# Kernel optimization log

Measured on AMD Instinct MI355X. Metric: run time of the kernel, lower is better.

Reference implementation:

```python
import jax, jax.numpy as jnp
import numpy as np

N_NODES = 100000
N_EDGES = 1250000
D_IN, D_HID, D_OUT = 64, 32, 41


def setup_inputs() -> dict:
    key = jax.random.key(0)
    ks = jax.random.split(key, 7)
    x = jax.random.normal(ks[0], (N_NODES, D_IN), dtype=jnp.float32)
    edge_index = jax.random.randint(ks[1], (2, N_EDGES), 0, N_NODES, dtype=jnp.int64)
    # PyG SAGEConv params: lin_l (applied to aggregated neighbors, has bias),
    # lin_r (applied to root, no bias). Stored here as [in, out] matrices.
    W1l = jax.random.normal(ks[2], (D_IN, D_HID), dtype=jnp.float32) / np.sqrt(D_IN)
    b1 = jnp.zeros((D_HID,), dtype=jnp.float32)
    W1r = jax.random.normal(ks[3], (D_IN, D_HID), dtype=jnp.float32) / np.sqrt(D_IN)
    W2l = jax.random.normal(ks[4], (D_HID, D_OUT), dtype=jnp.float32) / np.sqrt(D_HID)
    b2 = jnp.zeros((D_OUT,), dtype=jnp.float32)
    W2r = jax.random.normal(ks[5], (D_HID, D_OUT), dtype=jnp.float32) / np.sqrt(D_HID)
    return {"x": x, "edge_index": edge_index, "W1l": W1l, "b1": b1, "W1r": W1r,
            "W2l": W2l, "b2": b2, "W2r": W2r}


def _sage_conv(h, src, dst, n_nodes, Wl, b, Wr):
    # mean-aggregate source features at destination nodes (PyG default aggr='mean')
    msg = h[src]  # [E, d] irregular gather
    agg = jax.ops.segment_sum(msg, dst, num_segments=n_nodes)
    cnt = jax.ops.segment_sum(jnp.ones((src.shape[0],), dtype=h.dtype), dst,
                              num_segments=n_nodes)
    agg = agg / jnp.maximum(cnt, 1.0)[:, None]
    return agg @ Wl + b + h @ Wr


def reference(x, edge_index, W1l, b1, W1r, W2l, b2, W2r):
    src, dst = edge_index[0], edge_index[1]
    n = x.shape[0]
    h = _sage_conv(x, src, dst, n, W1l, b1, W1r)
    h = jax.nn.relu(h)
    # F.dropout(training=self.training) -> identity in eval/inference mode
    out = _sage_conv(h, src, dst, n, W2l, b2, W2r)
    return out
```

## Files before the change

kernel.cpp:

```cpp
#include <hip/hip_runtime.h>

#define N_NODES 100000
#define N_EDGES 1250000
#define D_IN 64
#define D_HID 32
#define D_OUT 41
#define NBUK 196
#define BSH 9
#define BCAP 6912
#define BBLK 512
#define BCHUNK 2442
#define PBLK 1563
#define ROWCAP 48
#define LSTR 88
#define ZERO_OFF 6400000

typedef short bf16x8 __attribute__((ext_vector_type(8)));
typedef float f32x4 __attribute__((ext_vector_type(4)));

__device__ __forceinline__ float bflo(unsigned int u) {
    union { unsigned int i; float f; } v; v.i = u << 16; return v.f;
}
__device__ __forceinline__ float bfhi(unsigned int u) {
    union { unsigned int i; float f; } v; v.i = u & 0xffff0000u; return v.f;
}
__device__ __forceinline__ unsigned short f2bf(float f) {
    union { float f; unsigned int i; } v; v.f = f;
    unsigned int x = v.i;
    return (unsigned short)((x + 0x7fffu + ((x >> 16) & 1u)) >> 16);
}
__device__ __forceinline__ void acc8(float* a, uint4 u) {
    a[0] += bflo(u.x); a[1] += bfhi(u.x);
    a[2] += bflo(u.y); a[3] += bfhi(u.y);
    a[4] += bflo(u.z); a[5] += bfhi(u.z);
    a[6] += bflo(u.w); a[7] += bfhi(u.w);
}

__global__ __launch_bounds__(256) void k_front(const int* __restrict__ src,
                                               const int* __restrict__ dst,
                                               unsigned int* __restrict__ bucket_cnt,
                                               unsigned int* __restrict__ buckets,
                                               const float* __restrict__ x,
                                               const float* __restrict__ W1l,
                                               const float* __restrict__ W1r,
                                               const float* __restrict__ b1,
                                               unsigned short* __restrict__ xl,
                                               unsigned short* __restrict__ xr) {
    __shared__ short smem[2 * 64 * LSTR];
    int tid = threadIdx.x;
    if (blockIdx.x < BBLK) {
        int* hist = (int*)smem;
        int* cur  = hist + NBUK;
        for (int i = tid; i < NBUK; i += 256)
            atomicCAS(&bucket_cnt[i], 0xAAAAAAAAu, 0u);
        for (int i = tid; i < NBUK; i += 256) hist[i] = 0;
        __syncthreads();
        int e0 = blockIdx.x * BCHUNK;
        int e1 = e0 + BCHUNK; if (e1 > N_EDGES) e1 = N_EDGES;
        int e = e0 + tid;
        for (; e + 768 < e1; e += 1024) {
            int t0 = dst[e];
            int t1 = dst[e + 256];
            int t2 = dst[e + 512];
            int t3 = dst[e + 768];
            atomicAdd(&hist[t0 >> BSH], 1);
            atomicAdd(&hist[t1 >> BSH], 1);
            atomicAdd(&hist[t2 >> BSH], 1);
            atomicAdd(&hist[t3 >> BSH], 1);
        }
        for (; e < e1; e += 256)
            atomicAdd(&hist[dst[e] >> BSH], 1);
        __syncthreads();
        for (int i = tid; i < NBUK; i += 256)
            cur[i] = (int)atomicAdd(&bucket_cnt[i], (unsigned int)hist[i]);
        __syncthreads();
        e = e0 + tid;
        for (; e + 768 < e1; e += 1024) {
            int t0 = dst[e],       s0 = src[e];
            int t1 = dst[e + 256], s1 = src[e + 256];
            int t2 = dst[e + 512], s2 = src[e + 512];
            int t3 = dst[e + 768], s3 = src[e + 768];
            int b0 = t0 >> BSH, p0 = atomicAdd(&cur[b0], 1);
            if (p0 < BCAP) buckets[(size_t)b0 * BCAP + p0] =
                (unsigned int)s0 | ((unsigned int)(t0 & 511) << 17);
            int b1i = t1 >> BSH, p1 = atomicAdd(&cur[b1i], 1);
            if (p1 < BCAP) buckets[(size_t)b1i * BCAP + p1] =
                (unsigned int)s1 | ((unsigned int)(t1 & 511) << 17);
            int b2 = t2 >> BSH, p2 = atomicAdd(&cur[b2], 1);
            if (p2 < BCAP) buckets[(size_t)b2 * BCAP + p2] =
                (unsigned int)s2 | ((unsigned int)(t2 & 511) << 17);
            int b3 = t3 >> BSH, p3 = atomicAdd(&cur[b3], 1);
            if (p3 < BCAP) buckets[(size_t)b3 * BCAP + p3] =
                (unsigned int)s3 | ((unsigned int)(t3 & 511) << 17);
        }
        for (; e < e1; e += 256) {
            int t = dst[e];
            int b = t >> BSH;
            int pos = atomicAdd(&cur[b], 1);
            if (pos < BCAP)
                buckets[(size_t)b * BCAP + pos] =
                    (unsigned int)src[e] | ((unsigned int)(t & 511) << 17);
        }
        return;
    }
    short* sX  = smem;
    short* sWT = smem + 64 * LSTR;
    int n0 = (blockIdx.x - BBLK) * 64;
    for (int i = tid; i < 64 * 64; i += 256) {
        int col = i >> 6, kk = i & 63;
        float v = (col < 32) ? W1l[kk * 32 + col] : W1r[kk * 32 + (col - 32)];
        sWT[col * LSTR + kk] = (short)f2bf(v);
    }
    {
        int g = tid >> 2, q = tid & 3;
        int n = n0 + g;
        short pk[16];
        if (n < N_NODES) {
            const float4* xr4 = (const float4*)(x + (size_t)n * D_IN + q * 16);
            float4 f0 = xr4[0], f1 = xr4[1], f2 = xr4[2], f3 = xr4[3];
            pk[0] = f2bf(f0.x); pk[1] = f2bf(f0.y); pk[2] = f2bf(f0.z); pk[3] = f2bf(f0.w);
            pk[4] = f2bf(f1.x); pk[5] = f2bf(f1.y); pk[6] = f2bf(f1.z); pk[7] = f2bf(f1.w);
            pk[8] = f2bf(f2.x); pk[9] = f2bf(f2.y); pk[10] = f2bf(f2.z); pk[11] = f2bf(f2.w);
            pk[12] = f2bf(f3.x); pk[13] = f2bf(f3.y); pk[14] = f2bf(f3.z); pk[15] = f2bf(f3.w);
        } else {
            for (int t = 0; t < 16; ++t) pk[t] = 0;
        }
        *(bf16x8*)(sX + g * LSTR + q * 16)     = *(bf16x8*)pk;
        *(bf16x8*)(sX + g * LSTR + q * 16 + 8) = *(bf16x8*)(pk + 8);
    }
    __syncthreads();
    int wid = tid >> 6, lane = tid & 63;
    int quad = lane >> 4, lc = lane & 15;
    int m0 = wid << 4;
    const short* sa = sX + (m0 + lc) * LSTR + quad * 8;
    bf16x8 af0 = *(const bf16x8*)(sa);
    bf16x8 af1 = *(const bf16x8*)(sa + 32);
#pragma unroll
    for (int t = 0; t < 4; ++t) {
        const short* sbp = sWT + (t * 16 + lc) * LSTR + quad * 8;
        bf16x8 bf0 = *(const bf16x8*)(sbp);
        bf16x8 bf1 = *(const bf16x8*)(sbp + 32);
        f32x4 acc = {0.f, 0.f, 0.f, 0.f};
        acc = __builtin_amdgcn_mfma_f32_16x16x32_bf16(af0, bf0, acc, 0, 0, 0);
        acc = __builtin_amdgcn_mfma_f32_16x16x32_bf16(af1, bf1, acc, 0, 0, 0);
        int col = t * 16 + lc;
        float bias = (col >= 32) ? b1[col - 32] : 0.f;
#pragma unroll
        for (int r = 0; r < 4; ++r) {
            int n = n0 + m0 + (quad << 2) + r;
            if (n < N_NODES) {
                if (col < 32) xl[(size_t)n * D_HID + col] = f2bf(acc[r]);
                else          xr[(size_t)n * D_HID + (col - 32)] = f2bf(acc[r] + bias);
            } else if (col < 32) {
                xl[(size_t)n * D_HID + col] = 0;
            }
        }
    }
}

__global__ __launch_bounds__(256) void k_fill2(const unsigned int* __restrict__ buckets,
                                               const unsigned int* __restrict__ bucket_cnt,
                                               int* __restrict__ cnt,
                                               int* __restrict__ padcsr) {
    __shared__ int lcnt[512];
    int b = blockIdx.x, tid = threadIdx.x;
    lcnt[tid] = 0; lcnt[tid + 256] = 0;
    __syncthreads();
    int total = (int)bucket_cnt[b]; if (total > BCAP) total = BCAP;
    const unsigned int* bk = buckets + (size_t)b * BCAP;
    int nbase = b << BSH;
    int i = tid;
    for (; i + 768 < total; i += 1024) {
        unsigned int w0 = bk[i];
        unsigned int w1 = bk[i + 256];
        unsigned int w2 = bk[i + 512];
        unsigned int w3 = bk[i + 768];
        int d0 = (int)(w0 >> 17), s0 = atomicAdd(&lcnt[d0], 1);
        if (s0 < ROWCAP) padcsr[(size_t)(nbase + d0) * ROWCAP + s0] = (int)((w0 & 0x1FFFFu) << 6);
        int d1 = (int)(w1 >> 17), s1 = atomicAdd(&lcnt[d1], 1);
        if (s1 < ROWCAP) padcsr[(size_t)(nbase + d1) * ROWCAP + s1] = (int)((w1 & 0x1FFFFu) << 6);
        int d2 = (int)(w2 >> 17), s2 = atomicAdd(&lcnt[d2], 1);
        if (s2 < ROWCAP) padcsr[(size_t)(nbase + d2) * ROWCAP + s2] = (int)((w2 & 0x1FFFFu) << 6);
        int d3 = (int)(w3 >> 17), s3 = atomicAdd(&lcnt[d3], 1);
        if (s3 < ROWCAP) padcsr[(size_t)(nbase + d3) * ROWCAP + s3] = (int)((w3 & 0x1FFFFu) << 6);
    }
    for (; i < total; i += 256) {
        unsigned int w = bk[i];
        int dl = (int)(w >> 17);
        int slot = atomicAdd(&lcnt[dl], 1);
        if (slot < ROWCAP)
            padcsr[(size_t)(nbase + dl) * ROWCAP + slot] = (int)((w & 0x1FFFFu) << 6);
    }
    __syncthreads();
#pragma unroll
    for (int half = 0; half < 2; ++half) {
        int li = tid + half * 256;
        int n = nbase + li;
        int c = lcnt[li];
        cnt[n] = c;
        int cc = c < ROWCAP ? c : ROWCAP;
        int ce = (cc + 15) & ~15; if (ce > ROWCAP) ce = ROWCAP;
        for (int s = cc; s < ce; ++s)
            padcsr[(size_t)n * ROWCAP + s] = ZERO_OFF;
    }
}

__global__ __launch_bounds__(256) void k_agg1(const int* __restrict__ padcsr,
                                              const int* __restrict__ cnt,
                                              const unsigned short* __restrict__ xl,
                                              const unsigned short* __restrict__ xr,
                                              unsigned short* __restrict__ h) {
    int tid = threadIdx.x;
    int g = tid >> 2, q = tid & 3;
    int n = blockIdx.x * 64 + g;
    int qb = q << 4;
    if (n >= N_NODES) {
        *(uint4*)((char*)h + ((size_t)n << 6) + qb) = make_uint4(0, 0, 0, 0);
        return;
    }
    int d = cnt[n];
    int dd = d < ROWCAP ? d : ROWCAP;
    int ddp = (dd + 15) & ~15; if (ddp > ROWCAP) ddp = ROWCAP;
    const int* row = padcsr + (size_t)n * ROWCAP;
    const char* xlb = (const char*)xl;
    float a[8] = {0.f, 0.f, 0.f, 0.f, 0.f, 0.f, 0.f, 0.f};
    for (int i = 0; i < ddp; i += 16) {
        int4 o0 = *(const int4*)(row + i);
        int4 o1 = *(const int4*)(row + i + 4);
        int4 o2 = *(const int4*)(row + i + 8);
        int4 o3 = *(const int4*)(row + i + 12);
        uint4 u0 = *(const uint4*)(xlb + o0.x + qb);
        uint4 u1 = *(const uint4*)(xlb + o0.y + qb);
        uint4 u2 = *(const uint4*)(xlb + o0.z + qb);
        uint4 u3 = *(const uint4*)(xlb + o0.w + qb);
        uint4 u4 = *(const uint4*)(xlb + o1.x + qb);
        uint4 u5 = *(const uint4*)(xlb + o1.y + qb);
        uint4 u6 = *(const uint4*)(xlb + o1.z + qb);
        uint4 u7 = *(const uint4*)(xlb + o1.w + qb);
        uint4 u8 = *(const uint4*)(xlb + o2.x + qb);
        uint4 u9 = *(const uint4*)(xlb + o2.y + qb);
        uint4 ua = *(const uint4*)(xlb + o2.z + qb);
        uint4 ub = *(const uint4*)(xlb + o2.w + qb);
        uint4 uc = *(const uint4*)(xlb + o3.x + qb);
        uint4 ud = *(const uint4*)(xlb + o3.y + qb);
        uint4 ue = *(const uint4*)(xlb + o3.z + qb);
        uint4 uf = *(const uint4*)(xlb + o3.w + qb);
        acc8(a, u0); acc8(a, u1); acc8(a, u2); acc8(a, u3);
        acc8(a, u4); acc8(a, u5); acc8(a, u6); acc8(a, u7);
        acc8(a, u8); acc8(a, u9); acc8(a, ua); acc8(a, ub);
        acc8(a, uc); acc8(a, ud); acc8(a, ue); acc8(a, uf);
    }
    float inv = 1.0f / fmaxf((float)d, 1.0f);
    uint4 r = *(const uint4*)((const char*)xr + ((size_t)n << 6) + qb);
    float o0 = fmaxf(a[0] * inv + bflo(r.x), 0.f);
    float o1 = fmaxf(a[1] * inv + bfhi(r.x), 0.f);
    float o2 = fmaxf(a[2] * inv + bflo(r.y), 0.f);
    float o3 = fmaxf(a[3] * inv + bfhi(r.y), 0.f);
    float o4 = fmaxf(a[4] * inv + bflo(r.z), 0.f);
    float o5 = fmaxf(a[5] * inv + bfhi(r.z), 0.f);
    float o6 = fmaxf(a[6] * inv + bflo(r.w), 0.f);
    float o7 = fmaxf(a[7] * inv + bfhi(r.w), 0.f);
    uint4 o;
    o.x = ((unsigned int)f2bf(o1) << 16) | f2bf(o0);
    o.y = ((unsigned int)f2bf(o3) << 16) | f2bf(o2);
    o.z = ((unsigned int)f2bf(o5) << 16) | f2bf(o4);
    o.w = ((unsigned int)f2bf(o7) << 16) | f2bf(o6);
    *(uint4*)((char*)h + ((size_t)n << 6) + qb) = o;
}

__global__ __launch_bounds__(256) void k_agg2out(const int* __restrict__ padcsr,
                                                 const int* __restrict__ cnt,
                                                 const unsigned short* __restrict__ h,
                                                 const float* __restrict__ W2l,
                                                 const float* __restrict__ b2,
                                                 const float* __restrict__ W2r,
                                                 float* __restrict__ out) {
    __shared__ short sA[64 * LSTR];
    __shared__ short sBT[48 * LSTR];
    int tid = threadIdx.x;
    int n0 = blockIdx.x * 64;
    for (int i = tid; i < 48 * 64; i += 256) {
        int col = i >> 6, kk = i & 63;
        float v = 0.f;
        if (col < D_OUT) v = (kk < 32) ? W2l[kk * D_OUT + col] : W2r[(kk - 32) * D_OUT + col];
        sBT[col * LSTR + kk] = (short)f2bf(v);
    }
    {
        int g = tid >> 2, q = tid & 3;
        int n = n0 + g;
        bool ok = (n < N_NODES);
        int qb = q << 4;
        int d = ok ? cnt[n] : 0;
        int dd = d < ROWCAP ? d : ROWCAP;
        int ddp = (dd + 15) & ~15; if (ddp > ROWCAP) ddp = ROWCAP;
        const int* row = padcsr + (size_t)n * ROWCAP;
        const char* hb = (const char*)h;
        float a[8] = {0.f, 0.f, 0.f, 0.f, 0.f, 0.f, 0.f, 0.f};
        for (int i = 0; i < ddp; i += 16) {
            int4 o0 = *(const int4*)(row + i);
            int4 o1 = *(const int4*)(row + i + 4);
            int4 o2 = *(const int4*)(row + i + 8);
            int4 o3 = *(const int4*)(row + i + 12);
            uint4 u0 = *(const uint4*)(hb + o0.x + qb);
            uint4 u1 = *(const uint4*)(hb + o0.y + qb);
            uint4 u2 = *(const uint4*)(hb + o0.z + qb);
            uint4 u3 = *(const uint4*)(hb + o0.w + qb);
            uint4 u4 = *(const uint4*)(hb + o1.x + qb);
            uint4 u5 = *(const uint4*)(hb + o1.y + qb);
            uint4 u6 = *(const uint4*)(hb + o1.z + qb);
            uint4 u7 = *(const uint4*)(hb + o1.w + qb);
            uint4 u8 = *(const uint4*)(hb + o2.x + qb);
            uint4 u9 = *(const uint4*)(hb + o2.y + qb);
            uint4 ua = *(const uint4*)(hb + o2.z + qb);
            uint4 ub = *(const uint4*)(hb + o2.w + qb);
            uint4 uc = *(const uint4*)(hb + o3.x + qb);
            uint4 ud = *(const uint4*)(hb + o3.y + qb);
            uint4 ue = *(const uint4*)(hb + o3.z + qb);
            uint4 uf = *(const uint4*)(hb + o3.w + qb);
            acc8(a, u0); acc8(a, u1); acc8(a, u2); acc8(a, u3);
            acc8(a, u4); acc8(a, u5); acc8(a, u6); acc8(a, u7);
            acc8(a, u8); acc8(a, u9); acc8(a, ua); acc8(a, ub);
            acc8(a, uc); acc8(a, ud); acc8(a, ue); acc8(a, uf);
        }
        float inv = 1.0f / fmaxf((float)d, 1.0f);
        short pk[8];
#pragma unroll
        for (int t = 0; t < 8; ++t) pk[t] = (short)f2bf(a[t] * inv);
        *(bf16x8*)(sA + g * LSTR + q * 8) = *(bf16x8*)pk;
        uint4 hr = ok ? *(const uint4*)(hb + ((size_t)n << 6) + qb)
                      : make_uint4(0, 0, 0, 0);
        *(uint4*)(sA + g * LSTR + 32 + q * 8) = hr;
    }
    __syncthreads();
    int wid = tid >> 6, lane = tid & 63;
    int quad = lane >> 4, lc = lane & 15;
    int m0 = wid << 4;
    const short* sa = sA + (m0 + lc) * LSTR + quad * 8;
    bf16x8 af0 = *(const bf16x8*)(sa);
    bf16x8 af1 = *(const bf16x8*)(sa + 32);
#pragma unroll
    for (int t = 0; t < 3; ++t) {
        const short* sbp = sBT + (t * 16 + lc) * LSTR + quad * 8;
        bf16x8 bf0 = *(const bf16x8*)(sbp);
        bf16x8 bf1 = *(const bf16x8*)(sbp + 32);
        f32x4 acc = {0.f, 0.f, 0.f, 0.f};
        acc = __builtin_amdgcn_mfma_f32_16x16x32_bf16(af0, bf0, acc, 0, 0, 0);
        acc = __builtin_amdgcn_mfma_f32_16x16x32_bf16(af1, bf1, acc, 0, 0, 0);
        int j = t * 16 + lc;
        if (j < D_OUT) {
            float bias = b2[j];
#pragma unroll
            for (int r = 0; r < 4; ++r) {
                int n = n0 + m0 + (quad << 2) + r;
                if (n < N_NODES) out[(size_t)n * D_OUT + j] = acc[r] + bias;
            }
        }
    }
}

extern "C" void kernel_launch(void* const* d_in, const int* in_sizes, int n_in,
                              void* d_out, int out_size, void* d_ws, size_t ws_size,
                              hipStream_t stream) {
    const float* x   = (const float*)d_in[0];
    const int*   ei  = (const int*)d_in[1];
    const int*   src = ei;
    const int*   dst = ei + N_EDGES;
    const float* W1l = (const float*)d_in[2];
    const float* b1  = (const float*)d_in[3];
    const float* W1r = (const float*)d_in[4];
    const float* W2l = (const float*)d_in[5];
    const float* b2  = (const float*)d_in[6];
    const float* W2r = (const float*)d_in[7];
    float* out = (float*)d_out;

    int* iws = (int*)d_ws;
    int* cnt        = iws;
    unsigned int* bucket_cnt = (unsigned int*)(iws + 100352);
    int* padcsr     = iws + 100608;
    unsigned int* buckets = (unsigned int*)(iws + 4917504);
    unsigned short* xl = (unsigned short*)(iws + 6272256);
    unsigned short* xr = (unsigned short*)(iws + 7872768);
    unsigned short* h  = (unsigned short*)(iws + 9473280);

    k_front<<<BBLK + PBLK, 256, 0, stream>>>(src, dst, bucket_cnt, buckets,
                                             x, W1l, W1r, b1, xl, xr);
    k_fill2<<<NBUK, 256, 0, stream>>>(buckets, bucket_cnt, cnt, padcsr);
    k_agg1<<<1563, 256, 0, stream>>>(padcsr, cnt, xl, xr, h);
    k_agg2out<<<1563, 256, 0, stream>>>(padcsr, cnt, h, W2l, b2, W2r, out);
}
```

Baseline: 189.5 us.

## Aggregate directly from dst buckets with LDS atomics, dropping padded CSR build

```diff
diff --git a/kernel.cpp b/kernel.cpp
--- a/kernel.cpp
+++ b/kernel.cpp
@@ -5,15 +5,14 @@
 #define D_IN 64
 #define D_HID 32
 #define D_OUT 41
-#define NBUK 196
-#define BSH 9
-#define BCAP 6912
-#define BBLK 512
-#define BCHUNK 2442
-#define PBLK 1563
-#define ROWCAP 48
+#define NBUK 784
+#define BSH 7
+#define BCAP 1920
+#define BBLK 192
+#define BCHUNK 6511
+#define PBLK 782
 #define LSTR 88
-#define ZERO_OFF 6400000
+#define ASTR 33
 
 typedef short bf16x8 __attribute__((ext_vector_type(8)));
 typedef float f32x4 __attribute__((ext_vector_type(4)));
@@ -29,11 +28,39 @@
     unsigned int x = v.i;
     return (unsigned short)((x + 0x7fffu + ((x >> 16) & 1u)) >> 16);
 }
-__device__ __forceinline__ void acc8(float* a, uint4 u) {
-    a[0] += bflo(u.x); a[1] += bfhi(u.x);
-    a[2] += bflo(u.y); a[3] += bfhi(u.y);
-    a[4] += bflo(u.z); a[5] += bfhi(u.z);
-    a[6] += bflo(u.w); a[7] += bfhi(u.w);
+
+__device__ __forceinline__ void ds_add8(float* accL, int* degL, unsigned int w,
+                                        uint4 u, int q) {
+    int dl = (int)(w >> 17);
+    float* p = accL + dl * ASTR + q * 8;
+    atomicAdd(p + 0, bflo(u.x)); atomicAdd(p + 1, bfhi(u.x));
+    atomicAdd(p + 2, bflo(u.y)); atomicAdd(p + 3, bfhi(u.y));
+    atomicAdd(p + 4, bflo(u.z)); atomicAdd(p + 5, bfhi(u.z));
+    atomicAdd(p + 6, bflo(u.w)); atomicAdd(p + 7, bfhi(u.w));
+    if (q == 0) atomicAdd(degL + dl, 1);
+}
+
+__device__ __forceinline__ void scan_accumulate(const unsigned int* bk, int total,
+                                                const char* tab, float* accL,
+                                                int* degL, int tid) {
+    int g = tid >> 2, q = tid & 3, qb = q << 4;
+    int t = g;
+    for (; t + 192 < total; t += 256) {
+        unsigned int w0 = bk[t], w1 = bk[t + 64], w2 = bk[t + 128], w3 = bk[t + 192];
+        uint4 u0 = *(const uint4*)(tab + ((w0 & 0x1FFFFu) << 6) + qb);
+        uint4 u1 = *(const uint4*)(tab + ((w1 & 0x1FFFFu) << 6) + qb);
+        uint4 u2 = *(const uint4*)(tab + ((w2 & 0x1FFFFu) << 6) + qb);
+        uint4 u3 = *(const uint4*)(tab + ((w3 & 0x1FFFFu) << 6) + qb);
+        ds_add8(accL, degL, w0, u0, q);
+        ds_add8(accL, degL, w1, u1, q);
+        ds_add8(accL, degL, w2, u2, q);
+        ds_add8(accL, degL, w3, u3, q);
+    }
+    for (; t < total; t += 64) {
+        unsigned int w = bk[t];
+        uint4 u = *(const uint4*)(tab + ((w & 0x1FFFFu) << 6) + qb);
+        ds_add8(accL, degL, w, u, q);
+    }
 }
 
 __global__ __launch_bounds__(256) void k_front(const int* __restrict__ src,
@@ -46,13 +73,11 @@
                                                const float* __restrict__ b1,
                                                unsigned short* __restrict__ xl,
                                                unsigned short* __restrict__ xr) {
-    __shared__ short smem[2 * 64 * LSTR];
+    __shared__ short smem[128 * LSTR + 64 * LSTR];
     int tid = threadIdx.x;
     if (blockIdx.x < BBLK) {
         int* hist = (int*)smem;
         int* cur  = hist + NBUK;
-        for (int i = tid; i < NBUK; i += 256)
-            atomicCAS(&bucket_cnt[i], 0xAAAAAAAAu, 0u);
         for (int i = tid; i < NBUK; i += 256) hist[i] = 0;
         __syncthreads();
         int e0 = blockIdx.x * BCHUNK;
@@ -72,7 +97,7 @@
             atomicAdd(&hist[dst[e] >> BSH], 1);
         __syncthreads();
         for (int i = tid; i < NBUK; i += 256)
-            cur[i] = (int)atomicAdd(&bucket_cnt[i], (unsigned int)hist[i]);
+            cur[i] = (int)atomicAdd(&bucket_cnt[i << 4], (unsigned int)hist[i]);
         __syncthreads();
         e = e0 + tid;
         for (; e + 768 < e1; e += 1024) {
@@ -82,16 +107,16 @@
             int t3 = dst[e + 768], s3 = src[e + 768];
             int b0 = t0 >> BSH, p0 = atomicAdd(&cur[b0], 1);
             if (p0 < BCAP) buckets[(size_t)b0 * BCAP + p0] =
-                (unsigned int)s0 | ((unsigned int)(t0 & 511) << 17);
+                (unsigned int)s0 | ((unsigned int)(t0 & 127) << 17);
             int b1i = t1 >> BSH, p1 = atomicAdd(&cur[b1i], 1);
             if (p1 < BCAP) buckets[(size_t)b1i * BCAP + p1] =
-                (unsigned int)s1 | ((unsigned int)(t1 & 511) << 17);
+                (unsigned int)s1 | ((unsigned int)(t1 & 127) << 17);
             int b2 = t2 >> BSH, p2 = atomicAdd(&cur[b2], 1);
             if (p2 < BCAP) buckets[(size_t)b2 * BCAP + p2] =
-                (unsigned int)s2 | ((unsigned int)(t2 & 511) << 17);
+                (unsigned int)s2 | ((unsigned int)(t2 & 127) << 17);
             int b3 = t3 >> BSH, p3 = atomicAdd(&cur[b3], 1);
             if (p3 < BCAP) buckets[(size_t)b3 * BCAP + p3] =
-                (unsigned int)s3 | ((unsigned int)(t3 & 511) << 17);
+                (unsigned int)s3 | ((unsigned int)(t3 & 127) << 17);
         }
         for (; e < e1; e += 256) {
             int t = dst[e];
@@ -99,262 +124,189 @@
             int pos = atomicAdd(&cur[b], 1);
             if (pos < BCAP)
                 buckets[(size_t)b * BCAP + pos] =
-                    (unsigned int)src[e] | ((unsigned int)(t & 511) << 17);
+                    (unsigned int)src[e] | ((unsigned int)(t & 127) << 17);
         }
         return;
     }
     short* sX  = smem;
-    short* sWT = smem + 64 * LSTR;
-    int n0 = (blockIdx.x - BBLK) * 64;
-    for (int i = tid; i < 64 * 64; i += 256) {
-        int col = i >> 6, kk = i & 63;
-        float v = (col < 32) ? W1l[kk * 32 + col] : W1r[kk * 32 + (col - 32)];
-        sWT[col * LSTR + kk] = (short)f2bf(v);
+    short* sWT = smem + 128 * LSTR;
+    int n0 = (blockIdx.x - BBLK) * 128;
+    for (int i = tid; i < 1024; i += 256) {
+        int k = i >> 4, c4 = i & 15;
+        float4 v = (c4 < 8) ? ((const float4*)W1l)[k * 8 + c4]
+                            : ((const float4*)W1r)[k * 8 + (c4 - 8)];
+        int col = c4 * 4;
+        sWT[(col + 0) * LSTR + k] = (short)f2bf(v.x);
+        sWT[(col + 1) * LSTR + k] = (short)f2bf(v.y);
+        sWT[(col + 2) * LSTR + k] = (short)f2bf(v.z);
+        sWT[(col + 3) * LSTR + k] = (short)f2bf(v.w);
     }
     {
-        int g = tid >> 2, q = tid & 3;
+        int g = tid >> 1, q2 = tid & 1;
         int n = n0 + g;
-        short pk[16];
+        short pk[32];
         if (n < N_NODES) {
-            const float4* xr4 = (const float4*)(x + (size_t)n * D_IN + q * 16);
-            float4 f0 = xr4[0], f1 = xr4[1], f2 = xr4[2], f3 = xr4[3];
-            pk[0] = f2bf(f0.x); pk[1] = f2bf(f0.y); pk[2] = f2bf(f0.z); pk[3] = f2bf(f0.w);
-            pk[4] = f2bf(f1.x); pk[5] = f2bf(f1.y); pk[6] = f2bf(f1.z); pk[7] = f2bf(f1.w);
-            pk[8] = f2bf(f2.x); pk[9] = f2bf(f2.y); pk[10] = f2bf(f2.z); pk[11] = f2bf(f2.w);
-            pk[12] = f2bf(f3.x); pk[13] = f2bf(f3.y); pk[14] = f2bf(f3.z); pk[15] = f2bf(f3.w);
+            const float4* xp = (const float4*)(x + (size_t)n * D_IN + q2 * 32);
+#pragma unroll
+            for (int i = 0; i < 8; ++i) {
+                float4 f = xp[i];
+                pk[i * 4 + 0] = (short)f2bf(f.x);
+                pk[i * 4 + 1] = (short)f2bf(f.y);
+                pk[i * 4 + 2] = (short)f2bf(f.z);
+                pk[i * 4 + 3] = (short)f2bf(f.w);
+            }
         } else {
-            for (int t = 0; t < 16; ++t) pk[t] = 0;
-        }
-        *(bf16x8*)(sX + g * LSTR + q * 16)     = *(bf16x8*)pk;
-        *(bf16x8*)(sX + g * LSTR + q * 16 + 8) = *(bf16x8*)(pk + 8);
+#pragma unroll
+            for (int i = 0; i < 32; ++i) pk[i] = 0;
+        }
+        short* sp = sX + g * LSTR + q2 * 32;
+        *(bf16x8*)(sp)      = *(bf16x8*)(pk);
+        *(bf16x8*)(sp + 8)  = *(bf16x8*)(pk + 8);
+        *(bf16x8*)(sp + 16) = *(bf16x8*)(pk + 16);
+        *(bf16x8*)(sp + 24) = *(bf16x8*)(pk + 24);
     }
     __syncthreads();
     int wid = tid >> 6, lane = tid & 63;
     int quad = lane >> 4, lc = lane & 15;
-    int m0 = wid << 4;
-    const short* sa = sX + (m0 + lc) * LSTR + quad * 8;
-    bf16x8 af0 = *(const bf16x8*)(sa);
-    bf16x8 af1 = *(const bf16x8*)(sa + 32);
-#pragma unroll
-    for (int t = 0; t < 4; ++t) {
-        const short* sbp = sWT + (t * 16 + lc) * LSTR + quad * 8;
-        bf16x8 bf0 = *(const bf16x8*)(sbp);
-        bf16x8 bf1 = *(const bf16x8*)(sbp + 32);
-        f32x4 acc = {0.f, 0.f, 0.f, 0.f};
-        acc = __builtin_amdgcn_mfma_f32_16x16x32_bf16(af0, bf0, acc, 0, 0, 0);
-        acc = __builtin_amdgcn_mfma_f32_16x16x32_bf16(af1, bf1, acc, 0, 0, 0);
-        int col = t * 16 + lc;
-        float bias = (col >= 32) ? b1[col - 32] : 0.f;
-#pragma unroll
-        for (int r = 0; r < 4; ++r) {
-            int n = n0 + m0 + (quad << 2) + r;
-            if (n < N_NODES) {
-                if (col < 32) xl[(size_t)n * D_HID + col] = f2bf(acc[r]);
-                else          xr[(size_t)n * D_HID + (col - 32)] = f2bf(acc[r] + bias);
-            } else if (col < 32) {
-                xl[(size_t)n * D_HID + col] = 0;
+#pragma unroll
+    for (int mm = 0; mm < 2; ++mm) {
+        int m0 = (wid + mm * 4) * 16;
+        const short* sa = sX + (m0 + lc) * LSTR + quad * 8;
+        bf16x8 af0 = *(const bf16x8*)(sa);
+        bf16x8 af1 = *(const bf16x8*)(sa + 32);
+#pragma unroll
+        for (int t = 0; t < 4; ++t) {
+            const short* sbp = sWT + (t * 16 + lc) * LSTR + quad * 8;
+            bf16x8 bf0 = *(const bf16x8*)(sbp);
+            bf16x8 bf1 = *(const bf16x8*)(sbp + 32);
+            f32x4 acc = {0.f, 0.f, 0.f, 0.f};
+            acc = __builtin_amdgcn_mfma_f32_16x16x32_bf16(af0, bf0, acc, 0, 0, 0);
+            acc = __builtin_amdgcn_mfma_f32_16x16x32_bf16(af1, bf1, acc, 0, 0, 0);
+            int col = t * 16 + lc;
+            float bias = (col >= 32) ? b1[col - 32] : 0.f;
+#pragma unroll
+            for (int r = 0; r < 4; ++r) {
+                int n = n0 + m0 + (quad << 2) + r;
+                if (n < N_NODES) {
+                    if (col < 32) xl[(size_t)n * D_HID + col] = f2bf(acc[r]);
+                    else          xr[(size_t)n * D_HID + (col - 32)] = f2bf(acc[r] + bias);
+                }
             }
         }
     }
 }
 
-__global__ __launch_bounds__(256) void k_fill2(const unsigned int* __restrict__ buckets,
+__global__ __launch_bounds__(256) void k_bagg1(const unsigned int* __restrict__ buckets,
                                                const unsigned int* __restrict__ bucket_cnt,
-                                               int* __restrict__ cnt,
-                                               int* __restrict__ padcsr) {
-    __shared__ int lcnt[512];
-    int b = blockIdx.x, tid = threadIdx.x;
-    lcnt[tid] = 0; lcnt[tid + 256] = 0;
-    __syncthreads();
-    int total = (int)bucket_cnt[b]; if (total > BCAP) total = BCAP;
-    const unsigned int* bk = buckets + (size_t)b * BCAP;
+                                               const unsigned short* __restrict__ xl,
+                                               const unsigned short* __restrict__ xr,
+                                               unsigned short* __restrict__ h) {
+    __shared__ float accL[128 * ASTR];
+    __shared__ int degL[128];
+    int tid = threadIdx.x, b = blockIdx.x;
+    for (int i = tid; i < 128 * ASTR; i += 256) accL[i] = 0.f;
+    if (tid < 128) degL[tid] = 0;
+    __syncthreads();
+    int total = (int)bucket_cnt[b << 4]; if (total > BCAP) total = BCAP;
+    scan_accumulate(buckets + (size_t)b * BCAP, total, (const char*)xl,
+                    accL, degL, tid);
+    __syncthreads();
     int nbase = b << BSH;
-    int i = tid;
-    for (; i + 768 < total; i += 1024) {
-        unsigned int w0 = bk[i];
-        unsigned int w1 = bk[i + 256];
-        unsigned int w2 = bk[i + 512];
-        unsigned int w3 = bk[i + 768];
-        int d0 = (int)(w0 >> 17), s0 = atomicAdd(&lcnt[d0], 1);
-        if (s0 < ROWCAP) padcsr[(size_t)(nbase + d0) * ROWCAP + s0] = (int)((w0 & 0x1FFFFu) << 6);
-        int d1 = (int)(w1 >> 17), s1 = atomicAdd(&lcnt[d1], 1);
-        if (s1 < ROWCAP) padcsr[(size_t)(nbase + d1) * ROWCAP + s1] = (int)((w1 & 0x1FFFFu) << 6);
-        int d2 = (int)(w2 >> 17), s2 = atomicAdd(&lcnt[d2], 1);
-        if (s2 < ROWCAP) padcsr[(size_t)(nbase + d2) * ROWCAP + s2] = (int)((w2 & 0x1FFFFu) << 6);
-        int d3 = (int)(w3 >> 17), s3 = atomicAdd(&lcnt[d3], 1);
-        if (s3 < ROWCAP) padcsr[(size_t)(nbase + d3) * ROWCAP + s3] = (int)((w3 & 0x1FFFFu) << 6);
-    }
-    for (; i < total; i += 256) {
-        unsigned int w = bk[i];
-        int dl = (int)(w >> 17);
-        int slot = atomicAdd(&lcnt[dl], 1);
-        if (slot < ROWCAP)
-            padcsr[(size_t)(nbase + dl) * ROWCAP + slot] = (int)((w & 0x1FFFFu) << 6);
-    }
-    __syncthreads();
-#pragma unroll
-    for (int half = 0; half < 2; ++half) {
-        int li = tid + half * 256;
+    int q = tid & 3, qb = q << 4;
+#pragma unroll
+    for (int r0 = 0; r0 < 2; ++r0) {
+        int li = (tid >> 2) + r0 * 64;
         int n = nbase + li;
-        int c = lcnt[li];
-        cnt[n] = c;
-        int cc = c < ROWCAP ? c : ROWCAP;
-        int ce = (cc + 15) & ~15; if (ce > ROWCAP) ce = ROWCAP;
-        for (int s = cc; s < ce; ++s)
-            padcsr[(size_t)n * ROWCAP + s] = ZERO_OFF;
-    }
-}
-
-__global__ __launch_bounds__(256) void k_agg1(const int* __restrict__ padcsr,
-                                              const int* __restrict__ cnt,
-                                              const unsigned short* __restrict__ xl,
-                                              const unsigned short* __restrict__ xr,
-                                              unsigned short* __restrict__ h) {
-    int tid = threadIdx.x;
-    int g = tid >> 2, q = tid & 3;
-    int n = blockIdx.x * 64 + g;
-    int qb = q << 4;
-    if (n >= N_NODES) {
-        *(uint4*)((char*)h + ((size_t)n << 6) + qb) = make_uint4(0, 0, 0, 0);
-        return;
-    }
-    int d = cnt[n];
-    int dd = d < ROWCAP ? d : ROWCAP;
-    int ddp = (dd + 15) & ~15; if (ddp > ROWCAP) ddp = ROWCAP;
-    const int* row = padcsr + (size_t)n * ROWCAP;
-    const char* xlb = (const char*)xl;
-    float a[8] = {0.f, 0.f, 0.f, 0.f, 0.f, 0.f, 0.f, 0.f};
-    for (int i = 0; i < ddp; i += 16) {
-        int4 o0 = *(const int4*)(row + i);
-        int4 o1 = *(const int4*)(row + i + 4);
-        int4 o2 = *(const int4*)(row + i + 8);
-        int4 o3 = *(const int4*)(row + i + 12);
-        uint4 u0 = *(const uint4*)(xlb + o0.x + qb);
-        uint4 u1 = *(const uint4*)(xlb + o0.y + qb);
-        uint4 u2 = *(const uint4*)(xlb + o0.z + qb);
-        uint4 u3 = *(const uint4*)(xlb + o0.w + qb);
-        uint4 u4 = *(const uint4*)(xlb + o1.x + qb);
-        uint4 u5 = *(const uint4*)(xlb + o1.y + qb);
-        uint4 u6 = *(const uint4*)(xlb + o1.z + qb);
-        uint4 u7 = *(const uint4*)(xlb + o1.w + qb);
-        uint4 u8 = *(const uint4*)(xlb + o2.x + qb);
-        uint4 u9 = *(const uint4*)(xlb + o2.y + qb);
-        uint4 ua = *(const uint4*)(xlb + o2.z + qb);
-        uint4 ub = *(const uint4*)(xlb + o2.w + qb);
-        uint4 uc = *(const uint4*)(xlb + o3.x + qb);
-        uint4 ud = *(const uint4*)(xlb + o3.y + qb);
-        uint4 ue = *(const uint4*)(xlb + o3.z + qb);
-        uint4 uf = *(const uint4*)(xlb + o3.w + qb);
-        acc8(a, u0); acc8(a, u1); acc8(a, u2); acc8(a, u3);
-        acc8(a, u4); acc8(a, u5); acc8(a, u6); acc8(a, u7);
-        acc8(a, u8); acc8(a, u9); acc8(a, ua); acc8(a, ub);
-        acc8(a, uc); acc8(a, ud); acc8(a, ue); acc8(a, uf);
-    }
-    float inv = 1.0f / fmaxf((float)d, 1.0f);
-    uint4 r = *(const uint4*)((const char*)xr + ((size_t)n << 6) + qb);
-    float o0 = fmaxf(a[0] * inv + bflo(r.x), 0.f);
-    float o1 = fmaxf(a[1] * inv + bfhi(r.x), 0.f);
-    float o2 = fmaxf(a[2] * inv + bflo(r.y), 0.f);
-    float o3 = fmaxf(a[3] * inv + bfhi(r.y), 0.f);
-    float o4 = fmaxf(a[4] * inv + bflo(r.z), 0.f);
-    float o5 = fmaxf(a[5] * inv + bfhi(r.z), 0.f);
-    float o6 = fmaxf(a[6] * inv + bflo(r.w), 0.f);
-    float o7 = fmaxf(a[7] * inv + bfhi(r.w), 0.f);
-    uint4 o;
-    o.x = ((unsigned int)f2bf(o1) << 16) | f2bf(o0);
-    o.y = ((unsigned int)f2bf(o3) << 16) | f2bf(o2);
-    o.z = ((unsigned int)f2bf(o5) << 16) | f2bf(o4);
-    o.w = ((unsigned int)f2bf(o7) << 16) | f2bf(o6);
-    *(uint4*)((char*)h + ((size_t)n << 6) + qb) = o;
-}
-
-__global__ __launch_bounds__(256) void k_agg2out(const int* __restrict__ padcsr,
-                                                 const int* __restrict__ cnt,
-                                                 const unsigned short* __restrict__ h,
-                                                 const float* __restrict__ W2l,
-                                                 const float* __restrict__ b2,
-                                                 const float* __restrict__ W2r,
-                                                 float* __restrict__ out) {
+        if (n < N_NODES) {
+            float inv = 1.0f / fmaxf((float)degL[li], 1.0f);
+            const float* ar = accL + li * ASTR + q * 8;
+            uint4 rr = *(const uint4*)((const char*)xr + ((size_t)n << 6) + qb);
+            float o0 = fmaxf(ar[0] * inv + bflo(rr.x), 0.f);
+            float o1 = fmaxf(ar[1] * inv + bfhi(rr.x), 0.f);
+            float o2 = fmaxf(ar[2] * inv + bflo(rr.y), 0.f);
+            float o3 = fmaxf(ar[3] * inv + bfhi(rr.y), 0.f);
+            float o4 = fmaxf(ar[4] * inv + bflo(rr.z), 0.f);
+            float o5 = fmaxf(ar[5] * inv + bfhi(rr.z), 0.f);
+            float o6 = fmaxf(ar[6] * inv + bflo(rr.w), 0.f);
+            float o7 = fmaxf(ar[7] * inv + bfhi(rr.w), 0.f);
+            uint4 o;
+            o.x = ((unsigned int)f2bf(o1) << 16) | f2bf(o0);
+            o.y = ((unsigned int)f2bf(o3) << 16) | f2bf(o2);
+            o.z = ((unsigned int)f2bf(o5) << 16) | f2bf(o4);
+            o.w = ((unsigned int)f2bf(o7) << 16) | f2bf(o6);
+            *(uint4*)((char*)h + ((size_t)n << 6) + qb) = o;
+        }
+    }
+}
+
+__global__ __launch_bounds__(256) void k_bagg2(const unsigned int* __restrict__ buckets,
+                                               const unsigned int* __restrict__ bucket_cnt,
+                                               const unsigned short* __restrict__ h,
+                                               const float* __restrict__ W2l,
+                                               const float* __restrict__ b2,
+                                               const float* __restrict__ W2r,
+                                               float* __restrict__ out) {
+    __shared__ float accL[128 * ASTR];
+    __shared__ int degL[128];
+    __shared__ short sBT[48 * LSTR];
     __shared__ short sA[64 * LSTR];
-    __shared__ short sBT[48 * LSTR];
-    int tid = threadIdx.x;
-    int n0 = blockIdx.x * 64;
+    int tid = threadIdx.x, b = blockIdx.x;
     for (int i = tid; i < 48 * 64; i += 256) {
         int col = i >> 6, kk = i & 63;
         float v = 0.f;
         if (col < D_OUT) v = (kk < 32) ? W2l[kk * D_OUT + col] : W2r[(kk - 32) * D_OUT + col];
         sBT[col * LSTR + kk] = (short)f2bf(v);
     }
-    {
-        int g = tid >> 2, q = tid & 3;
-        int n = n0 + g;
-        bool ok = (n < N_NODES);
-        int qb = q << 4;
-        int d = ok ? cnt[n] : 0;
-        int dd = d < ROWCAP ? d : ROWCAP;
-        int ddp = (dd + 15) & ~15; if (ddp > ROWCAP) ddp = ROWCAP;
-        const int* row = padcsr + (size_t)n * ROWCAP;
-        const char* hb = (const char*)h;
-        float a[8] = {0.f, 0.f, 0.f, 0.f, 0.f, 0.f, 0.f, 0.f};
-        for (int i = 0; i < ddp; i += 16) {
-            int4 o0 = *(const int4*)(row + i);
-            int4 o1 = *(const int4*)(row + i + 4);
-            int4 o2 = *(const int4*)(row + i + 8);
-            int4 o3 = *(const int4*)(row + i + 12);
-            uint4 u0 = *(const uint4*)(hb + o0.x + qb);
-            uint4 u1 = *(const uint4*)(hb + o0.y + qb);
-            uint4 u2 = *(const uint4*)(hb + o0.z + qb);
-            uint4 u3 = *(const uint4*)(hb + o0.w + qb);
-            uint4 u4 = *(const uint4*)(hb + o1.x + qb);
-            uint4 u5 = *(const uint4*)(hb + o1.y + qb);
-            uint4 u6 = *(const uint4*)(hb + o1.z + qb);
-            uint4 u7 = *(const uint4*)(hb + o1.w + qb);
-            uint4 u8 = *(const uint4*)(hb + o2.x + qb);
-            uint4 u9 = *(const uint4*)(hb + o2.y + qb);
-            uint4 ua = *(const uint4*)(hb + o2.z + qb);
-            uint4 ub = *(const uint4*)(hb + o2.w + qb);
-            uint4 uc = *(const uint4*)(hb + o3.x + qb);
-            uint4 ud = *(const uint4*)(hb + o3.y + qb);
-            uint4 ue = *(const uint4*)(hb + o3.z + qb);
-            uint4 uf = *(const uint4*)(hb + o3.w + qb);
-            acc8(a, u0); acc8(a, u1); acc8(a, u2); acc8(a, u3);
-            acc8(a, u4); acc8(a, u5); acc8(a, u6); acc8(a, u7);
-            acc8(a, u8); acc8(a, u9); acc8(a, ua); acc8(a, ub);
-            acc8(a, uc); acc8(a, ud); acc8(a, ue); acc8(a, uf);
-        }
-        float inv = 1.0f / fmaxf((float)d, 1.0f);
-        short pk[8];
-#pragma unroll
-        for (int t = 0; t < 8; ++t) pk[t] = (short)f2bf(a[t] * inv);
-        *(bf16x8*)(sA + g * LSTR + q * 8) = *(bf16x8*)pk;
-        uint4 hr = ok ? *(const uint4*)(hb + ((size_t)n << 6) + qb)
-                      : make_uint4(0, 0, 0, 0);
-        *(uint4*)(sA + g * LSTR + 32 + q * 8) = hr;
-    }
-    __syncthreads();
+    for (int i = tid; i < 128 * ASTR; i += 256) accL[i] = 0.f;
+    if (tid < 128) degL[tid] = 0;
+    __syncthreads();
+    int total = (int)bucket_cnt[b << 4]; if (total > BCAP) total = BCAP;
+    const char* hb = (const char*)h;
+    scan_accumulate(buckets + (size_t)b * BCAP, total, hb, accL, degL, tid);
+    __syncthreads();
+    int nbase = b << BSH;
     int wid = tid >> 6, lane = tid & 63;
     int quad = lane >> 4, lc = lane & 15;
-    int m0 = wid << 4;
-    const short* sa = sA + (m0 + lc) * LSTR + quad * 8;
-    bf16x8 af0 = *(const bf16x8*)(sa);
-    bf16x8 af1 = *(const bf16x8*)(sa + 32);
-#pragma unroll
-    for (int t = 0; t < 3; ++t) {
-        const short* sbp = sBT + (t * 16 + lc) * LSTR + quad * 8;
-        bf16x8 bf0 = *(const bf16x8*)(sbp);
-        bf16x8 bf1 = *(const bf16x8*)(sbp + 32);
-        f32x4 acc = {0.f, 0.f, 0.f, 0.f};
-        acc = __builtin_amdgcn_mfma_f32_16x16x32_bf16(af0, bf0, acc, 0, 0, 0);
-        acc = __builtin_amdgcn_mfma_f32_16x16x32_bf16(af1, bf1, acc, 0, 0, 0);
-        int j = t * 16 + lc;
-        if (j < D_OUT) {
-            float bias = b2[j];
-#pragma unroll
-            for (int r = 0; r < 4; ++r) {
-                int n = n0 + m0 + (quad << 2) + r;
-                if (n < N_NODES) out[(size_t)n * D_OUT + j] = acc[r] + bias;
+#pragma unroll
+    for (int sub = 0; sub < 2; ++sub) {
+        {
+            int li = sub * 64 + (tid >> 2);
+            int q = tid & 3, qb = q << 4;
+            int n = nbase + li;
+            float inv = 1.0f / fmaxf((float)degL[li], 1.0f);
+            const float* ar = accL + li * ASTR + q * 8;
+            short pk[8];
+#pragma unroll
+            for (int j = 0; j < 8; ++j) pk[j] = (short)f2bf(ar[j] * inv);
+            uint4 hr = (n < N_NODES) ? *(const uint4*)(hb + ((size_t)n << 6) + qb)
+                                     : make_uint4(0, 0, 0, 0);
+            short* sp = sA + (tid >> 2) * LSTR + q * 8;
+            *(bf16x8*)(sp)      = *(bf16x8*)pk;
+            *(uint4*)(sp + 32)  = hr;
+        }
+        __syncthreads();
+        const short* sa = sA + (wid * 16 + lc) * LSTR + quad * 8;
+        bf16x8 af0 = *(const bf16x8*)(sa);
+        bf16x8 af1 = *(const bf16x8*)(sa + 32);
+#pragma unroll
+        for (int t = 0; t < 3; ++t) {
+            const short* sbp = sBT + (t * 16 + lc) * LSTR + quad * 8;
+            bf16x8 bf0 = *(const bf16x8*)(sbp);
+            bf16x8 bf1 = *(const bf16x8*)(sbp + 32);
+            f32x4 acc = {0.f, 0.f, 0.f, 0.f};
+            acc = __builtin_amdgcn_mfma_f32_16x16x32_bf16(af0, bf0, acc, 0, 0, 0);
+            acc = __builtin_amdgcn_mfma_f32_16x16x32_bf16(af1, bf1, acc, 0, 0, 0);
+            int j = t * 16 + lc;
+            if (j < D_OUT) {
+                float bias = b2[j];
+#pragma unroll
+                for (int r = 0; r < 4; ++r) {
+                    int n = nbase + sub * 64 + wid * 16 + (quad << 2) + r;
+                    if (n < N_NODES) out[(size_t)n * D_OUT + j] = acc[r] + bias;
+                }
             }
         }
+        __syncthreads();
     }
 }
 
@@ -374,17 +326,15 @@
     float* out = (float*)d_out;
 
     int* iws = (int*)d_ws;
-    int* cnt        = iws;
-    unsigned int* bucket_cnt = (unsigned int*)(iws + 100352);
-    int* padcsr     = iws + 100608;
-    unsigned int* buckets = (unsigned int*)(iws + 4917504);
-    unsigned short* xl = (unsigned short*)(iws + 6272256);
-    unsigned short* xr = (unsigned short*)(iws + 7872768);
-    unsigned short* h  = (unsigned short*)(iws + 9473280);
-
+    unsigned int* bucket_cnt = (unsigned int*)iws;
+    unsigned int* buckets = (unsigned int*)(iws + 12544);
+    unsigned short* xl = (unsigned short*)(iws + 1517824);
+    unsigned short* xr = (unsigned short*)(iws + 3123456);
+    unsigned short* h  = (unsigned short*)(iws + 4729088);
+
+    hipMemsetAsync(bucket_cnt, 0, NBUK * 16 * sizeof(int), stream);
     k_front<<<BBLK + PBLK, 256, 0, stream>>>(src, dst, bucket_cnt, buckets,
                                              x, W1l, W1r, b1, xl, xr);
-    k_fill2<<<NBUK, 256, 0, stream>>>(buckets, bucket_cnt, cnt, padcsr);
-    k_agg1<<<1563, 256, 0, stream>>>(padcsr, cnt, xl, xr, h);
-    k_agg2out<<<1563, 256, 0, stream>>>(padcsr, cnt, h, W2l, b2, W2r, out);
-}
+    k_bagg1<<<NBUK, 256, 0, stream>>>(buckets, bucket_cnt, xl, xr, h);
+    k_bagg2<<<NBUK, 256, 0, stream>>>(buckets, bucket_cnt, h, W2l, b2, W2r, out);
+}
```

After: 649.9 us. 243% more time.
